# Optimization experiments

Measured on AMD Instinct MI355X. Metric: run time of the kernel, lower is better.

## Reference

```python
import jax, jax.numpy as jnp
import numpy as np

N_NODES = 50000
N_EDGES = 600000
D = 128
EDGE_D = 32
N_LAYERS = 3
BN_EPS = 1e-5


def setup_inputs() -> dict:
    key = jax.random.key(0)
    ks = jax.random.split(key, 8)
    x = jax.random.normal(ks[0], (N_NODES, D), dtype=jnp.float32)
    edge_index = jax.random.randint(ks[1], (2, N_EDGES), 0, N_NODES, dtype=jnp.int64)
    edge_attr = jax.random.normal(ks[2], (N_EDGES, EDGE_D), dtype=jnp.float32)
    W_lin = jax.random.normal(ks[3], (N_LAYERS, EDGE_D, D), dtype=jnp.float32) * 0.05
    b_lin = jnp.zeros((N_LAYERS, D), dtype=jnp.float32)
    W1 = jax.random.normal(ks[4], (N_LAYERS, D, D), dtype=jnp.float32) * 0.05
    b1 = jnp.zeros((N_LAYERS, D), dtype=jnp.float32)
    W2 = jax.random.normal(ks[5], (N_LAYERS, D, D), dtype=jnp.float32) * 0.05
    b2 = jnp.zeros((N_LAYERS, D), dtype=jnp.float32)
    gamma = jnp.ones((N_LAYERS, D), dtype=jnp.float32)
    beta = jnp.zeros((N_LAYERS, D), dtype=jnp.float32)
    return {"x": x, "edge_index": edge_index, "edge_attr": edge_attr,
            "W_lin": W_lin, "b_lin": b_lin, "W1": W1, "b1": b1,
            "W2": W2, "b2": b2, "gamma": gamma, "beta": beta}


def reference(x, edge_index, edge_attr, W_lin, b_lin, W1, b1, W2, b2, gamma, beta):
    # MPNN with GINEConv layers: for each layer,
    #   msg_e = ReLU(x[src_e] + Linear(edge_attr_e))      (PyG GINEConv edge lift)
    #   agg_i = sum over edges with dst==i of msg_e        (scatter-sum)
    #   h     = MLP((1+eps)*x + agg), eps=0
    #   x     = ReLU(BatchNorm1d(h))                       (training-mode batch stats)
    src, dst = edge_index[0], edge_index[1]
    n = x.shape[0]
    for l in range(W1.shape[0]):
        e = edge_attr @ W_lin[l] + b_lin[l]                 # [E, D]
        msg = jax.nn.relu(x[src] + e)                       # gather + fuse
        agg = jax.ops.segment_sum(msg, dst, num_segments=n)  # [N, D]
        h = x + agg                                         # eps = 0
        h = jax.nn.relu(h @ W1[l] + b1[l]) @ W2[l] + b2[l]   # GIN MLP
        mu = jnp.mean(h, axis=0)
        var = jnp.var(h, axis=0)
        h = (h - mu) * jax.lax.rsqrt(var + BN_EPS) * gamma[l] + beta[l]
        x = jax.nn.relu(h)
    return x
```

## Files before the change

kernel.cpp:

```cpp
#include <hip/hip_runtime.h>

#define D_DIM 128
#define EDGE_DIM 32
#define BN_EPS 1e-5f

typedef __attribute__((ext_vector_type(8))) _Float16 f16x8;
typedef __attribute__((ext_vector_type(2))) _Float16 half2v;
typedef __attribute__((ext_vector_type(4))) float f32x4;
typedef unsigned short ushort_t;

__device__ __forceinline__ unsigned short f2h(float f) {
    union { _Float16 h; unsigned short u; } c;
    c.h = (_Float16)f;
    return c.u;
}
__device__ __forceinline__ unsigned pk2h(float lo, float hi) {
    return (unsigned)f2h(lo) | ((unsigned)f2h(hi) << 16);
}
__device__ __forceinline__ half2v asH2(unsigned u) {
    union { unsigned u; half2v h; } c;
    c.u = u;
    return c.h;
}
__device__ __forceinline__ float fdot2f(half2v a, half2v b, float c) {
#if __has_builtin(__builtin_amdgcn_fdot2)
    return __builtin_amdgcn_fdot2(a, b, c, false);
#else
    return c + (float)a.x * (float)b.x + (float)a.y * (float)b.y;
#endif
}

__global__ __launch_bounds__(256) void hist_kernel(
    const int* __restrict__ dst, int* __restrict__ cnt, int E)
{
    for (int e = blockIdx.x * 256 + threadIdx.x; e < E; e += gridDim.x * 256)
        atomicAdd(&cnt[dst[e]], 1);
}

__global__ __launch_bounds__(256) void scan_local_kernel(
    const int* __restrict__ cnt, int* __restrict__ off,
    int* __restrict__ blksum, int n)
{
    __shared__ int part[256];
    const int t = threadIdx.x;
    const int base = blockIdx.x * 2048 + t * 8;
    int v[8];
    int s = 0;
#pragma unroll
    for (int j = 0; j < 8; ++j) {
        const int idx = base + j;
        const int c = (idx < n) ? cnt[idx] : 0;
        v[j] = s;
        s += c;
    }
    part[t] = s;
    __syncthreads();
    for (int d = 1; d < 256; d <<= 1) {
        const int val = (t >= d) ? part[t - d] : 0;
        __syncthreads();
        part[t] += val;
        __syncthreads();
    }
    const int texcl = (t > 0) ? part[t - 1] : 0;
#pragma unroll
    for (int j = 0; j < 8; ++j) {
        const int idx = base + j;
        if (idx < n) off[idx] = texcl + v[j];
    }
    if (t == 255) blksum[blockIdx.x] = part[255];
}

__global__ __launch_bounds__(64) void scan_tops_kernel(
    int* __restrict__ blksum, int* __restrict__ off, int n, int B)
{
    if (threadIdx.x == 0) {
        int run = 0;
        for (int b = 0; b < B; ++b) {
            const int v = blksum[b];
            blksum[b] = run;
            run += v;
        }
        off[n] = run;
    }
}

__global__ __launch_bounds__(256) void scan_add_kernel(
    int* __restrict__ off, int* __restrict__ cur,
    const int* __restrict__ blksum, int n)
{
    const int base = blockIdx.x * 2048;
    const int add = blksum[blockIdx.x];
    for (int j = threadIdx.x; j < 2048; j += 256) {
        const int i = base + j;
        if (i < n) {
            const int v = off[i] + add;
            off[i] = v;
            cur[i] = v;
        }
    }
}

__global__ __launch_bounds__(256) void scatter_conv_kernel(
    const int* __restrict__ src, const int* __restrict__ dst,
    const float* __restrict__ ea,
    int* __restrict__ cur, int* __restrict__ srcs,
    uint4* __restrict__ ea16q, int E)
{
    for (int e = blockIdx.x * 256 + threadIdx.x; e < E; e += gridDim.x * 256) {
        const int p = atomicAdd(&cur[dst[e]], 1);
        srcs[p] = src[e];
        const float* __restrict__ er = ea + (size_t)e * EDGE_DIM;
#pragma unroll
        for (int q = 0; q < 4; ++q) {
            const float4 a = *(const float4*)(er + q * 8);
            const float4 b = *(const float4*)(er + q * 8 + 4);
            uint4 o;
            o.x = pk2h(a.x, a.y); o.y = pk2h(a.z, a.w);
            o.z = pk2h(b.x, b.y); o.w = pk2h(b.z, b.w);
            ea16q[(size_t)p * 4 + q] = o;
        }
    }
}

__global__ __launch_bounds__(256) void wl_build_kernel(
    const float* __restrict__ Wl, unsigned* __restrict__ wl16d)
{
#pragma unroll
    for (int r = 0; r < 8; ++r) {
        const int idx = r * 256 + threadIdx.x;
        const int kp = idx >> 7, c = idx & 127;
        wl16d[idx] = pk2h(Wl[(2 * kp) * D_DIM + c], Wl[(2 * kp + 1) * D_DIM + c]);
    }
}

__global__ __launch_bounds__(256) void xprep0_kernel(
    const float* __restrict__ h, uint2* __restrict__ x16q, int M)
{
    const int total = M * 32;
    for (int i = blockIdx.x * 256 + threadIdx.x; i < total; i += gridDim.x * 256) {
        const float4 v = ((const float4*)h)[i];
        uint2 o; o.x = pk2h(v.x, v.y); o.y = pk2h(v.z, v.w);
        x16q[i] = o;
    }
}

template<int OUTF32>
__global__ __launch_bounds__(256) void apply_kernel(
    const ushort_t* __restrict__ h16, const float* __restrict__ scsh,
    uint2* __restrict__ x16q, float* __restrict__ outp, int M)
{
    __shared__ float sc[128], sh[128];
    if (threadIdx.x < 128) {
        sc[threadIdx.x] = scsh[threadIdx.x];
        sh[threadIdx.x] = scsh[128 + threadIdx.x];
    }
    __syncthreads();
    const int total = M * 32;
    for (int i = blockIdx.x * 256 + threadIdx.x; i < total; i += gridDim.x * 256) {
        const uint2 hv = *(const uint2*)(h16 + (size_t)i * 4);
        const half2v a = asH2(hv.x), b = asH2(hv.y);
        const int c = (i & 31) * 4;
        const float v0 = fmaxf(fmaf((float)a.x, sc[c + 0], sh[c + 0]), 0.f);
        const float v1 = fmaxf(fmaf((float)a.y, sc[c + 1], sh[c + 1]), 0.f);
        const float v2 = fmaxf(fmaf((float)b.x, sc[c + 2], sh[c + 2]), 0.f);
        const float v3 = fmaxf(fmaf((float)b.y, sc[c + 3], sh[c + 3]), 0.f);
        if (OUTF32) {
            f32x4 o = {v0, v1, v2, v3};
            *(f32x4*)(outp + (size_t)i * 4) = o;
        } else {
            uint2 o; o.x = pk2h(v0, v1); o.y = pk2h(v2, v3);
            x16q[i] = o;
        }
    }
}

__global__ __launch_bounds__(256) void edge_agg_kernel(
    const unsigned* __restrict__ x16d,
    const int*      __restrict__ srcs,
    const uint4*    __restrict__ ea16q,
    const int*      __restrict__ row_off,
    const unsigned* __restrict__ wl16d,
    const float*    __restrict__ bl,
    float*          __restrict__ agg,
    int nNodes)
{
    const int lane = threadIdx.x & 63;
    const int wid  = threadIdx.x >> 6;

    unsigned wA[16], wB[16];
#pragma unroll
    for (int kp = 0; kp < 16; ++kp) {
        const uint2 w2 = *(const uint2*)(wl16d + kp * 128 + 2 * lane);
        wA[kp] = w2.x; wB[kp] = w2.y;
    }
    const float b0 = bl[2 * lane];
    const float b1 = bl[2 * lane + 1];

    const int stride = gridDim.x * 4;
    for (int node = blockIdx.x * 4 + wid; node < nNodes; node += stride) {
        const int beg = __builtin_amdgcn_readfirstlane(row_off[node]);
        const int end = __builtin_amdgcn_readfirstlane(row_off[node + 1]);
        float acc0 = 0.f, acc1 = 0.f;

        auto edge_body = [&](int p) {
            const int s = srcs[p];
            const uint4 q0 = ea16q[(size_t)p * 4 + 0];
            const uint4 q1 = ea16q[(size_t)p * 4 + 1];
            const uint4 q2 = ea16q[(size_t)p * 4 + 2];
            const uint4 q3 = ea16q[(size_t)p * 4 + 3];
            const unsigned xd = x16d[(size_t)s * 64 + lane];
            const unsigned aw[16] = {q0.x, q0.y, q0.z, q0.w,
                                     q1.x, q1.y, q1.z, q1.w,
                                     q2.x, q2.y, q2.z, q2.w,
                                     q3.x, q3.y, q3.z, q3.w};
            float e0 = b0, e1 = b1;
#pragma unroll
            for (int kp = 0; kp < 16; ++kp) {
                e0 = fdot2f(asH2(aw[kp]), asH2(wA[kp]), e0);
                e1 = fdot2f(asH2(aw[kp]), asH2(wB[kp]), e1);
            }
            const half2v xh = asH2(xd);
            acc0 += fmaxf((float)xh.x + e0, 0.f);
            acc1 += fmaxf((float)xh.y + e1, 0.f);
        };

        int j = beg;
        const int head = (end - beg) & 3;
#pragma unroll 1
        for (int t = 0; t < head; ++t) { edge_body(j); ++j; }
#pragma unroll 1
        for (; j < end; j += 4) {
            edge_body(j);
            edge_body(j + 1);
            edge_body(j + 2);
            edge_body(j + 3);
        }
        *(float2*)(agg + (size_t)node * D_DIM + 2 * lane) = make_float2(acc0, acc1);
    }
}

__global__ __launch_bounds__(256) void fused_mlp_kernel(
    const unsigned* __restrict__ x16d,
    const float* __restrict__ agg,
    const float* __restrict__ W1,
    const float* __restrict__ b1,
    const float* __restrict__ W2,
    const float* __restrict__ b2,
    ushort_t* __restrict__ h16,
    float* __restrict__ sums,
    int M)
{
    __shared__ char ATb[128 * 256];
    __shared__ char WTb[128 * 256];
    __shared__ float bsum[256];
    const int tid = threadIdx.x;
    const int m0  = blockIdx.x * 128;

    bsum[tid] = 0.f;

#pragma unroll
    for (int i = 0; i < 16; ++i) {
        const int idx = i * 256 + tid;
        const int r = idx >> 5, c4 = idx & 31;
        const int row = m0 + r;
        f32x4 v = {0.f, 0.f, 0.f, 0.f};
        if (row < M) {
            const uint2 xv = *(const uint2*)(x16d + (size_t)row * 64 + c4 * 2);
            const f32x4 g  = *(const f32x4*)(agg + (size_t)row * 128 + c4 * 4);
            const half2v xa = asH2(xv.x), xb = asH2(xv.y);
            v[0] = (float)xa.x + g[0];
            v[1] = (float)xa.y + g[1];
            v[2] = (float)xb.x + g[2];
            v[3] = (float)xb.y + g[3];
        }
        uint2 p; p.x = pk2h(v[0], v[1]); p.y = pk2h(v[2], v[3]);
        *(uint2*)(ATb + r * 256 + ((c4 * 8) ^ ((r & 7) << 4))) = p;
    }
#pragma unroll
    for (int i = 0; i < 8; ++i) {
        const int c4 = (tid >> 6) + 4 * i;
        const int kp = tid & 63;
        const f32x4 wa = *(const f32x4*)(W1 + (size_t)(2 * kp) * 128 + c4 * 4);
        const f32x4 wb = *(const f32x4*)(W1 + (size_t)(2 * kp + 1) * 128 + c4 * 4);
#pragma unroll
        for (int j = 0; j < 4; ++j) {
            const int col = c4 * 4 + j;
            *(unsigned*)(WTb + col * 256 + ((kp * 4) ^ ((col & 7) << 4))) = pk2h(wa[j], wb[j]);
        }
    }
    __syncthreads();

    const int lane = tid & 63;
    const int w    = tid >> 6;
    const int fr   = lane & 15;
    const int fg   = lane >> 4;
    const int ar0  = w * 32 + fr;
    const int asz  = (ar0 & 7) << 4;

    f32x4 acc[2][8];
#pragma unroll
    for (int a = 0; a < 2; ++a)
#pragma unroll
        for (int b = 0; b < 8; ++b) acc[a][b] = (f32x4){0.f, 0.f, 0.f, 0.f};

#pragma unroll
    for (int ks = 0; ks < 4; ++ks) {
        const int kb = ks * 64 + fg * 16;
        const f16x8 a0 = *(const f16x8*)(ATb + ar0 * 256 + (kb ^ asz));
        const f16x8 a1 = *(const f16x8*)(ATb + (ar0 + 16) * 256 + (kb ^ asz));
#pragma unroll
        for (int cb = 0; cb < 8; ++cb) {
            const int col = cb * 16 + fr;
            const f16x8 b = *(const f16x8*)(WTb + col * 256 + (kb ^ ((col & 7) << 4)));
            acc[0][cb] = __builtin_amdgcn_mfma_f32_16x16x32_f16(a0, b, acc[0][cb], 0, 0, 0);
            acc[1][cb] = __builtin_amdgcn_mfma_f32_16x16x32_f16(a1, b, acc[1][cb], 0, 0, 0);
        }
    }
    __syncthreads();

    {
        float b1v[8];
#pragma unroll
        for (int cb = 0; cb < 8; ++cb) b1v[cb] = b1[cb * 16 + fr];
#pragma unroll
        for (int rf = 0; rf < 2; ++rf) {
            const int rb = w * 32 + rf * 16 + fg * 4;
#pragma unroll
            for (int cb = 0; cb < 8; ++cb) {
                const int c = cb * 16 + fr;
#pragma unroll
                for (int j = 0; j < 4; ++j) {
                    const int r = rb + j;
                    const float v = fmaxf(acc[rf][cb][j] + b1v[cb], 0.f);
                    *(ushort_t*)(ATb + r * 256 + ((c * 2) ^ ((r & 7) << 4))) = f2h(v);
                }
            }
        }
    }
#pragma unroll
    for (int i = 0; i < 8; ++i) {
        const int c4 = (tid >> 6) + 4 * i;
        const int kp = tid & 63;
        const f32x4 wa = *(const f32x4*)(W2 + (size_t)(2 * kp) * 128 + c4 * 4);
        const f32x4 wb = *(const f32x4*)(W2 + (size_t)(2 * kp + 1) * 128 + c4 * 4);
#pragma unroll
        for (int j = 0; j < 4; ++j) {
            const int col = c4 * 4 + j;
            *(unsigned*)(WTb + col * 256 + ((kp * 4) ^ ((col & 7) << 4))) = pk2h(wa[j], wb[j]);
        }
    }
#pragma unroll
    for (int a = 0; a < 2; ++a)
#pragma unroll
        for (int b = 0; b < 8; ++b) acc[a][b] = (f32x4){0.f, 0.f, 0.f, 0.f};
    __syncthreads();

#pragma unroll
    for (int ks = 0; ks < 4; ++ks) {
        const int kb = ks * 64 + fg * 16;
        const f16x8 a0 = *(const f16x8*)(ATb + ar0 * 256 + (kb ^ asz));
        const f16x8 a1 = *(const f16x8*)(ATb + (ar0 + 16) * 256 + (kb ^ asz));
#pragma unroll
        for (int cb = 0; cb < 8; ++cb) {
            const int col = cb * 16 + fr;
            const f16x8 b = *(const f16x8*)(WTb + col * 256 + (kb ^ ((col & 7) << 4)));
            acc[0][cb] = __builtin_amdgcn_mfma_f32_16x16x32_f16(a0, b, acc[0][cb], 0, 0, 0);
            acc[1][cb] = __builtin_amdgcn_mfma_f32_16x16x32_f16(a1, b, acc[1][cb], 0, 0, 0);
        }
    }

    float b2v[8];
#pragma unroll
    for (int cb = 0; cb < 8; ++cb) b2v[cb] = b2[cb * 16 + fr];
    float s[8], q[8];
#pragma unroll
    for (int cb = 0; cb < 8; ++cb) { s[cb] = 0.f; q[cb] = 0.f; }

#pragma unroll
    for (int rf = 0; rf < 2; ++rf) {
        const int r0 = m0 + w * 32 + rf * 16 + fg * 4;
#pragma unroll
        for (int cb = 0; cb < 8; ++cb) {
            const int col = cb * 16 + fr;
#pragma unroll
            for (int j = 0; j < 4; ++j) {
                const int row = r0 + j;
                if (row < M) {
                    const float v = acc[rf][cb][j] + b2v[cb];
                    h16[(size_t)row * 128 + col] = f2h(v);
                    s[cb] += v;
                    q[cb] += v * v;
                }
            }
        }
    }
#pragma unroll
    for (int cb = 0; cb < 8; ++cb) {
        float ss = s[cb]; ss += __shfl_down(ss, 32); ss += __shfl_down(ss, 16);
        float qq = q[cb]; qq += __shfl_down(qq, 32); qq += __shfl_down(qq, 16);
        if (lane < 16) {
            atomicAdd(&bsum[cb * 16 + lane], ss);
            atomicAdd(&bsum[128 + cb * 16 + lane], qq);
        }
    }
    __syncthreads();
    unsafeAtomicAdd(&sums[tid], bsum[tid]);
}

__global__ __launch_bounds__(128) void bn_finalize_kernel(
    const float* __restrict__ sums,
    const float* __restrict__ gamma, const float* __restrict__ beta,
    float* __restrict__ scsh, float invM)
{
    const int c = threadIdx.x;
    const float mu  = sums[c] * invM;
    const float var = sums[128 + c] * invM - mu * mu;
    const float sc  = gamma[c] * rsqrtf(var + BN_EPS);
    scsh[c]       = sc;
    scsh[128 + c] = beta[c] - mu * sc;
}

extern "C" void kernel_launch(void* const* d_in, const int* in_sizes, int n_in,
                              void* d_out, int out_size, void* d_ws, size_t ws_size,
                              hipStream_t stream)
{
    const float* x_in  = (const float*)d_in[0];
    const int*   ei    = (const int*)  d_in[1];
    const float* ea    = (const float*)d_in[2];
    const float* W_lin = (const float*)d_in[3];
    const float* b_lin = (const float*)d_in[4];
    const float* W1    = (const float*)d_in[5];
    const float* b1    = (const float*)d_in[6];
    const float* W2    = (const float*)d_in[7];
    const float* b2    = (const float*)d_in[8];
    const float* gamma = (const float*)d_in[9];
    const float* beta  = (const float*)d_in[10];

    const int N = in_sizes[0] / D_DIM;
    const int E = in_sizes[2] / EDGE_DIM;
    const int L = in_sizes[3] / (EDGE_DIM * D_DIM);

    const int* src = ei;
    const int* dst = ei + E;

    float* out = (float*)d_out;

    char* wp = (char*)d_ws;
    auto take = [&wp](size_t bytes) {
        char* r = wp;
        wp += (bytes + 15) & ~(size_t)15;
        return r;
    };
    float*     agg     = (float*)    take((size_t)N * D_DIM * 4);
    ushort_t*  h16     = (ushort_t*) take((size_t)N * D_DIM * 2);
    unsigned*  x16d    = (unsigned*) take((size_t)N * D_DIM * 2);
    float*     sums    = (float*)    take(256 * 4);
    float*     scsh    = (float*)    take(256 * 4);
    unsigned*  wl16d   = (unsigned*) take(16 * 128 * 4);
    int*       cnt     = (int*)      take((size_t)N * 4);
    int*       row_off = (int*)      take((size_t)(N + 1) * 4);
    int*       cur     = (int*)      take((size_t)N * 4);
    int*       blksum  = (int*)      take(256 * 4);
    int*       srcs    = (int*)      take((size_t)E * 4);
    uint4*     ea16q   = (uint4*)    take((size_t)E * 64);

    const int gemmBlocks = (N + 127) / 128;
    const int scanBlocks = (N + 2047) / 2048;

    hipMemsetAsync(cnt, 0, (size_t)N * sizeof(int), stream);
    hist_kernel<<<1024, 256, 0, stream>>>(dst, cnt, E);
    scan_local_kernel<<<scanBlocks, 256, 0, stream>>>(cnt, row_off, blksum, N);
    scan_tops_kernel<<<1, 64, 0, stream>>>(blksum, row_off, N, scanBlocks);
    scan_add_kernel<<<scanBlocks, 256, 0, stream>>>(row_off, cur, blksum, N);
    scatter_conv_kernel<<<1024, 256, 0, stream>>>(src, dst, ea, cur, srcs, ea16q, E);

    for (int l = 0; l < L; ++l) {
        hipMemsetAsync(sums, 0, 256 * sizeof(float), stream);

        const float* Wl_l = W_lin + (size_t)l * EDGE_DIM * D_DIM;
        const float* bl_l = b_lin + (size_t)l * D_DIM;
        const float* W1_l = W1 + (size_t)l * D_DIM * D_DIM;
        const float* b1_l = b1 + (size_t)l * D_DIM;
        const float* W2_l = W2 + (size_t)l * D_DIM * D_DIM;
        const float* b2_l = b2 + (size_t)l * D_DIM;

        if (l == 0)
            xprep0_kernel<<<1024, 256, 0, stream>>>(x_in, (uint2*)x16d, N);
        else
            apply_kernel<0><<<1024, 256, 0, stream>>>(h16, scsh, (uint2*)x16d, nullptr, N);

        wl_build_kernel<<<1, 256, 0, stream>>>(Wl_l, wl16d);

        edge_agg_kernel<<<2048, 256, 0, stream>>>(
            x16d, srcs, ea16q, row_off, wl16d, bl_l, agg, N);

        fused_mlp_kernel<<<gemmBlocks, 256, 0, stream>>>(
            x16d, agg, W1_l, b1_l, W2_l, b2_l, h16, sums, N);

        bn_finalize_kernel<<<1, 128, 0, stream>>>(
            sums, gamma + (size_t)l * D_DIM, beta + (size_t)l * D_DIM,
            scsh, 1.f / (float)N);
    }

    apply_kernel<1><<<1024, 256, 0, stream>>>(h16, scsh, nullptr, out, N);
}
```

Before: 433.1 us.

## Compute edge linear with MFMA per edge chunk and scatter via segmented atomics

```diff
diff --git a/kernel.cpp b/kernel.cpp
--- a/kernel.cpp
+++ b/kernel.cpp
@@ -3,6 +3,7 @@
 #define D_DIM 128
 #define EDGE_DIM 32
 #define BN_EPS 1e-5f
+#define CHUNK 128
 
 typedef __attribute__((ext_vector_type(8))) _Float16 f16x8;
 typedef __attribute__((ext_vector_type(2))) _Float16 half2v;
@@ -21,13 +22,6 @@
     union { unsigned u; half2v h; } c;
     c.u = u;
     return c.h;
-}
-__device__ __forceinline__ float fdot2f(half2v a, half2v b, float c) {
-#if __has_builtin(__builtin_amdgcn_fdot2)
-    return __builtin_amdgcn_fdot2(a, b, c, false);
-#else
-    return c + (float)a.x * (float)b.x + (float)a.y * (float)b.y;
-#endif
 }
 
 __global__ __launch_bounds__(256) void hist_kernel(
@@ -103,12 +97,14 @@
 __global__ __launch_bounds__(256) void scatter_conv_kernel(
     const int* __restrict__ src, const int* __restrict__ dst,
     const float* __restrict__ ea,
-    int* __restrict__ cur, int* __restrict__ srcs,
+    int* __restrict__ cur, int* __restrict__ srcs, int* __restrict__ dsts,
     uint4* __restrict__ ea16q, int E)
 {
     for (int e = blockIdx.x * 256 + threadIdx.x; e < E; e += gridDim.x * 256) {
-        const int p = atomicAdd(&cur[dst[e]], 1);
+        const int d = dst[e];
+        const int p = atomicAdd(&cur[d], 1);
         srcs[p] = src[e];
+        dsts[p] = d;
         const float* __restrict__ er = ea + (size_t)e * EDGE_DIM;
 #pragma unroll
         for (int q = 0; q < 4; ++q) {
@@ -122,32 +118,48 @@
     }
 }
 
-__global__ __launch_bounds__(256) void wl_build_kernel(
-    const float* __restrict__ Wl, unsigned* __restrict__ wl16d)
-{
-#pragma unroll
-    for (int r = 0; r < 8; ++r) {
-        const int idx = r * 256 + threadIdx.x;
-        const int kp = idx >> 7, c = idx & 127;
-        wl16d[idx] = pk2h(Wl[(2 * kp) * D_DIM + c], Wl[(2 * kp + 1) * D_DIM + c]);
+__global__ __launch_bounds__(256) void wbuild_kernel(
+    const float* __restrict__ Wl, const float* __restrict__ W1f,
+    const float* __restrict__ W2f,
+    unsigned* __restrict__ wflin, unsigned* __restrict__ wf1d,
+    unsigned* __restrict__ wf2d)
+{
+    const int idx = blockIdx.x * 256 + threadIdx.x;
+    if (idx < 2048) {
+        const int slot = idx >> 2, q = idx & 3;
+        const int cb = slot >> 6, lane = slot & 63;
+        const int col = cb * 16 + (lane & 15);
+        const int k0 = (lane >> 4) * 8 + 2 * q;
+        wflin[idx] = pk2h(Wl[k0 * D_DIM + col], Wl[(k0 + 1) * D_DIM + col]);
+    } else if (idx < 10240) {
+        const int i = idx - 2048;
+        const int col = i >> 6, kp = i & 63;
+        wf1d[i] = pk2h(W1f[(2 * kp) * D_DIM + col], W1f[(2 * kp + 1) * D_DIM + col]);
+    } else if (idx < 18432) {
+        const int i = idx - 10240;
+        const int col = i >> 6, kp = i & 63;
+        wf2d[i] = pk2h(W2f[(2 * kp) * D_DIM + col], W2f[(2 * kp + 1) * D_DIM + col]);
     }
 }
 
 __global__ __launch_bounds__(256) void xprep0_kernel(
-    const float* __restrict__ h, uint2* __restrict__ x16q, int M)
+    const float* __restrict__ h, uint2* __restrict__ x16q,
+    float* __restrict__ aggf, int M)
 {
     const int total = M * 32;
     for (int i = blockIdx.x * 256 + threadIdx.x; i < total; i += gridDim.x * 256) {
         const float4 v = ((const float4*)h)[i];
         uint2 o; o.x = pk2h(v.x, v.y); o.y = pk2h(v.z, v.w);
         x16q[i] = o;
+        ((float4*)aggf)[i] = v;
     }
 }
 
 template<int OUTF32>
 __global__ __launch_bounds__(256) void apply_kernel(
     const ushort_t* __restrict__ h16, const float* __restrict__ scsh,
-    uint2* __restrict__ x16q, float* __restrict__ outp, int M)
+    uint2* __restrict__ x16q, float* __restrict__ aggf,
+    float* __restrict__ outp, int M)
 {
     __shared__ float sc[128], sh[128];
     if (threadIdx.x < 128) {
@@ -170,88 +182,139 @@
         } else {
             uint2 o; o.x = pk2h(v0, v1); o.y = pk2h(v2, v3);
             x16q[i] = o;
-        }
-    }
-}
-
-__global__ __launch_bounds__(256) void edge_agg_kernel(
+            f32x4 g = {v0, v1, v2, v3};
+            *(f32x4*)(aggf + (size_t)i * 4) = g;
+        }
+    }
+}
+
+__global__ __launch_bounds__(256) void fused_edge_kernel(
     const unsigned* __restrict__ x16d,
     const int*      __restrict__ srcs,
-    const uint4*    __restrict__ ea16q,
-    const int*      __restrict__ row_off,
-    const unsigned* __restrict__ wl16d,
+    const int*      __restrict__ dsts,
+    const ushort_t* __restrict__ ea16,
+    const ushort_t* __restrict__ wflin,
     const float*    __restrict__ bl,
     float*          __restrict__ agg,
-    int nNodes)
-{
-    const int lane = threadIdx.x & 63;
-    const int wid  = threadIdx.x >> 6;
-
-    unsigned wA[16], wB[16];
-#pragma unroll
-    for (int kp = 0; kp < 16; ++kp) {
-        const uint2 w2 = *(const uint2*)(wl16d + kp * 128 + 2 * lane);
-        wA[kp] = w2.x; wB[kp] = w2.y;
-    }
-    const float b0 = bl[2 * lane];
-    const float b1 = bl[2 * lane + 1];
-
-    const int stride = gridDim.x * 4;
-    for (int node = blockIdx.x * 4 + wid; node < nNodes; node += stride) {
-        const int beg = __builtin_amdgcn_readfirstlane(row_off[node]);
-        const int end = __builtin_amdgcn_readfirstlane(row_off[node + 1]);
-        float acc0 = 0.f, acc1 = 0.f;
-
-        auto edge_body = [&](int p) {
-            const int s = srcs[p];
-            const uint4 q0 = ea16q[(size_t)p * 4 + 0];
-            const uint4 q1 = ea16q[(size_t)p * 4 + 1];
-            const uint4 q2 = ea16q[(size_t)p * 4 + 2];
-            const uint4 q3 = ea16q[(size_t)p * 4 + 3];
-            const unsigned xd = x16d[(size_t)s * 64 + lane];
-            const unsigned aw[16] = {q0.x, q0.y, q0.z, q0.w,
-                                     q1.x, q1.y, q1.z, q1.w,
-                                     q2.x, q2.y, q2.z, q2.w,
-                                     q3.x, q3.y, q3.z, q3.w};
-            float e0 = b0, e1 = b1;
-#pragma unroll
-            for (int kp = 0; kp < 16; ++kp) {
-                e0 = fdot2f(asH2(aw[kp]), asH2(wA[kp]), e0);
-                e1 = fdot2f(asH2(aw[kp]), asH2(wB[kp]), e1);
+    int E)
+{
+    __shared__ ushort_t eT[CHUNK * 132];
+    const int tid  = threadIdx.x;
+    const int lane = tid & 63;
+    const int w    = tid >> 6;
+    const int fr   = lane & 15;
+    const int fg   = lane >> 4;
+
+    f16x8 bfr[8];
+#pragma unroll
+    for (int cb = 0; cb < 8; ++cb)
+        bfr[cb] = *(const f16x8*)(wflin + (cb * 64 + lane) * 8);
+    float blv[8];
+#pragma unroll
+    for (int cb = 0; cb < 8; ++cb) blv[cb] = bl[cb * 16 + fr];
+
+    const size_t chunk0 = (size_t)blockIdx.x * CHUNK;
+#pragma unroll
+    for (int rr = 0; rr < 2; ++rr) {
+        const int rb = w * 2 + rr;
+        const f16x8 af = *(const f16x8*)(ea16 + (chunk0 + rb * 16 + fr) * 32 + fg * 8);
+        f32x4 acc[8];
+#pragma unroll
+        for (int cb = 0; cb < 8; ++cb) {
+            const f32x4 z = {0.f, 0.f, 0.f, 0.f};
+            acc[cb] = __builtin_amdgcn_mfma_f32_16x16x32_f16(af, bfr[cb], z, 0, 0, 0);
+        }
+#pragma unroll
+        for (int cb = 0; cb < 8; ++cb) {
+            const int col = cb * 16 + fr;
+#pragma unroll
+            for (int j = 0; j < 4; ++j) {
+                const int er = rb * 16 + fg * 4 + j;
+                eT[er * 132 + col] = f2h(acc[cb][j] + blv[cb]);
             }
-            const half2v xh = asH2(xd);
-            acc0 += fmaxf((float)xh.x + e0, 0.f);
-            acc1 += fmaxf((float)xh.y + e1, 0.f);
-        };
-
-        int j = beg;
-        const int head = (end - beg) & 3;
+        }
+    }
+    __syncthreads();
+
+    const int base = (int)chunk0 + w * 32;
+    int nE = E - base;
+    if (nE <= 0) return;
+    if (nE > 32) nE = 32;
+    const int pend = base + nE;
+
+    float a0 = 0.f, a1 = 0.f;
+    int p = base;
+
+    auto flush = [&](int d) {
+        unsafeAtomicAdd(&agg[(size_t)d * D_DIM + 2 * lane],     a0);
+        unsafeAtomicAdd(&agg[(size_t)d * D_DIM + 2 * lane + 1], a1);
+        a0 = 0.f; a1 = 0.f;
+    };
+
 #pragma unroll 1
-        for (int t = 0; t < head; ++t) { edge_body(j); ++j; }
+    for (; p + 3 < pend; p += 4) {
+        const int s0 = __builtin_amdgcn_readfirstlane(srcs[p]);
+        const int s1 = __builtin_amdgcn_readfirstlane(srcs[p + 1]);
+        const int s2 = __builtin_amdgcn_readfirstlane(srcs[p + 2]);
+        const int s3 = __builtin_amdgcn_readfirstlane(srcs[p + 3]);
+        const unsigned x0 = x16d[(size_t)s0 * 64 + lane];
+        const unsigned x1 = x16d[(size_t)s1 * 64 + lane];
+        const unsigned x2 = x16d[(size_t)s2 * 64 + lane];
+        const unsigned x3 = x16d[(size_t)s3 * 64 + lane];
+        const int ei = p - (int)chunk0;
+        const unsigned e0 = *(const unsigned*)&eT[(ei + 0) * 132 + 2 * lane];
+        const unsigned e1 = *(const unsigned*)&eT[(ei + 1) * 132 + 2 * lane];
+        const unsigned e2 = *(const unsigned*)&eT[(ei + 2) * 132 + 2 * lane];
+        const unsigned e3 = *(const unsigned*)&eT[(ei + 3) * 132 + 2 * lane];
+        const int d0 = __builtin_amdgcn_readfirstlane(dsts[p]);
+        const int d1 = __builtin_amdgcn_readfirstlane(dsts[p + 1]);
+        const int d2 = __builtin_amdgcn_readfirstlane(dsts[p + 2]);
+        const int d3 = __builtin_amdgcn_readfirstlane(dsts[p + 3]);
+        const int d4 = (p + 4 < pend) ? __builtin_amdgcn_readfirstlane(dsts[p + 4]) : -1;
+
+        { const half2v xh = asH2(x0), eh = asH2(e0);
+          a0 += fmaxf((float)xh.x + (float)eh.x, 0.f);
+          a1 += fmaxf((float)xh.y + (float)eh.y, 0.f);
+          if (d0 != d1) flush(d0); }
+        { const half2v xh = asH2(x1), eh = asH2(e1);
+          a0 += fmaxf((float)xh.x + (float)eh.x, 0.f);
+          a1 += fmaxf((float)xh.y + (float)eh.y, 0.f);
+          if (d1 != d2) flush(d1); }
+        { const half2v xh = asH2(x2), eh = asH2(e2);
+          a0 += fmaxf((float)xh.x + (float)eh.x, 0.f);
+          a1 += fmaxf((float)xh.y + (float)eh.y, 0.f);
+          if (d2 != d3) flush(d2); }
+        { const half2v xh = asH2(x3), eh = asH2(e3);
+          a0 += fmaxf((float)xh.x + (float)eh.x, 0.f);
+          a1 += fmaxf((float)xh.y + (float)eh.y, 0.f);
+          if (d3 != d4) flush(d3); }
+    }
 #pragma unroll 1
-        for (; j < end; j += 4) {
-            edge_body(j);
-            edge_body(j + 1);
-            edge_body(j + 2);
-            edge_body(j + 3);
-        }
-        *(float2*)(agg + (size_t)node * D_DIM + 2 * lane) = make_float2(acc0, acc1);
+    for (; p < pend; ++p) {
+        const int s = __builtin_amdgcn_readfirstlane(srcs[p]);
+        const unsigned xd = x16d[(size_t)s * 64 + lane];
+        const int ei = p - (int)chunk0;
+        const unsigned ed = *(const unsigned*)&eT[ei * 132 + 2 * lane];
+        const int d  = __builtin_amdgcn_readfirstlane(dsts[p]);
+        const int dn = (p + 1 < pend) ? __builtin_amdgcn_readfirstlane(dsts[p + 1]) : -1;
+        const half2v xh = asH2(xd), eh = asH2(ed);
+        a0 += fmaxf((float)xh.x + (float)eh.x, 0.f);
+        a1 += fmaxf((float)xh.y + (float)eh.y, 0.f);
+        if (d != dn) flush(d);
     }
 }
 
 __global__ __launch_bounds__(256) void fused_mlp_kernel(
-    const unsigned* __restrict__ x16d,
     const float* __restrict__ agg,
-    const float* __restrict__ W1,
+    const ushort_t* __restrict__ wf1,
     const float* __restrict__ b1,
-    const float* __restrict__ W2,
+    const ushort_t* __restrict__ wf2,
     const float* __restrict__ b2,
     ushort_t* __restrict__ h16,
     float* __restrict__ sums,
     int M)
 {
     __shared__ char ATb[128 * 256];
-    __shared__ char WTb[128 * 256];
     __shared__ float bsum[256];
     const int tid = threadIdx.x;
     const int m0  = blockIdx.x * 128;
@@ -264,29 +327,9 @@
         const int r = idx >> 5, c4 = idx & 31;
         const int row = m0 + r;
         f32x4 v = {0.f, 0.f, 0.f, 0.f};
-        if (row < M) {
-            const uint2 xv = *(const uint2*)(x16d + (size_t)row * 64 + c4 * 2);
-            const f32x4 g  = *(const f32x4*)(agg + (size_t)row * 128 + c4 * 4);
-            const half2v xa = asH2(xv.x), xb = asH2(xv.y);
-            v[0] = (float)xa.x + g[0];
-            v[1] = (float)xa.y + g[1];
-            v[2] = (float)xb.x + g[2];
-            v[3] = (float)xb.y + g[3];
-        }
-        uint2 p; p.x = pk2h(v[0], v[1]); p.y = pk2h(v[2], v[3]);
-        *(uint2*)(ATb + r * 256 + ((c4 * 8) ^ ((r & 7) << 4))) = p;
-    }
-#pragma unroll
-    for (int i = 0; i < 8; ++i) {
-        const int c4 = (tid >> 6) + 4 * i;
-        const int kp = tid & 63;
-        const f32x4 wa = *(const f32x4*)(W1 + (size_t)(2 * kp) * 128 + c4 * 4);
-        const f32x4 wb = *(const f32x4*)(W1 + (size_t)(2 * kp + 1) * 128 + c4 * 4);
-#pragma unroll
-        for (int j = 0; j < 4; ++j) {
-            const int col = c4 * 4 + j;
-            *(unsigned*)(WTb + col * 256 + ((kp * 4) ^ ((col & 7) << 4))) = pk2h(wa[j], wb[j]);
-        }
+        if (row < M) v = *(const f32x4*)(agg + (size_t)row * 128 + c4 * 4);
+        uint2 pk; pk.x = pk2h(v[0], v[1]); pk.y = pk2h(v[2], v[3]);
+        *(uint2*)(ATb + r * 256 + ((c4 * 8) ^ ((r & 7) << 4))) = pk;
     }
     __syncthreads();
 
@@ -308,12 +351,14 @@
         const int kb = ks * 64 + fg * 16;
         const f16x8 a0 = *(const f16x8*)(ATb + ar0 * 256 + (kb ^ asz));
         const f16x8 a1 = *(const f16x8*)(ATb + (ar0 + 16) * 256 + (kb ^ asz));
+        f16x8 bf[8];
+#pragma unroll
+        for (int cb = 0; cb < 8; ++cb)
+            bf[cb] = *(const f16x8*)(wf1 + (cb * 16 + fr) * 128 + ks * 32 + fg * 8);
 #pragma unroll
         for (int cb = 0; cb < 8; ++cb) {
-            const int col = cb * 16 + fr;
-            const f16x8 b = *(const f16x8*)(WTb + col * 256 + (kb ^ ((col & 7) << 4)));
-            acc[0][cb] = __builtin_amdgcn_mfma_f32_16x16x32_f16(a0, b, acc[0][cb], 0, 0, 0);
-            acc[1][cb] = __builtin_amdgcn_mfma_f32_16x16x32_f16(a1, b, acc[1][cb], 0, 0, 0);
+            acc[0][cb] = __builtin_amdgcn_mfma_f32_16x16x32_f16(a0, bf[cb], acc[0][cb], 0, 0, 0);
+            acc[1][cb] = __builtin_amdgcn_mfma_f32_16x16x32_f16(a1, bf[cb], acc[1][cb], 0, 0, 0);
         }
     }
     __syncthreads();
@@ -338,18 +383,6 @@
         }
     }
 #pragma unroll
-    for (int i = 0; i < 8; ++i) {
-        const int c4 = (tid >> 6) + 4 * i;
-        const int kp = tid & 63;
-        const f32x4 wa = *(const f32x4*)(W2 + (size_t)(2 * kp) * 128 + c4 * 4);
-        const f32x4 wb = *(const f32x4*)(W2 + (size_t)(2 * kp + 1) * 128 + c4 * 4);
-#pragma unroll
-        for (int j = 0; j < 4; ++j) {
-            const int col = c4 * 4 + j;
-            *(unsigned*)(WTb + col * 256 + ((kp * 4) ^ ((col & 7) << 4))) = pk2h(wa[j], wb[j]);
-        }
-    }
-#pragma unroll
     for (int a = 0; a < 2; ++a)
 #pragma unroll
         for (int b = 0; b < 8; ++b) acc[a][b] = (f32x4){0.f, 0.f, 0.f, 0.f};
@@ -360,12 +393,14 @@
         const int kb = ks * 64 + fg * 16;
         const f16x8 a0 = *(const f16x8*)(ATb + ar0 * 256 + (kb ^ asz));
         const f16x8 a1 = *(const f16x8*)(ATb + (ar0 + 16) * 256 + (kb ^ asz));
+        f16x8 bf[8];
+#pragma unroll
+        for (int cb = 0; cb < 8; ++cb)
+            bf[cb] = *(const f16x8*)(wf2 + (cb * 16 + fr) * 128 + ks * 32 + fg * 8);
 #pragma unroll
         for (int cb = 0; cb < 8; ++cb) {
-            const int col = cb * 16 + fr;
-            const f16x8 b = *(const f16x8*)(WTb + col * 256 + (kb ^ ((col & 7) << 4)));
-            acc[0][cb] = __builtin_amdgcn_mfma_f32_16x16x32_f16(a0, b, acc[0][cb], 0, 0, 0);
-            acc[1][cb] = __builtin_amdgcn_mfma_f32_16x16x32_f16(a1, b, acc[1][cb], 0, 0, 0);
+            acc[0][cb] = __builtin_amdgcn_mfma_f32_16x16x32_f16(a0, bf[cb], acc[0][cb], 0, 0, 0);
+            acc[1][cb] = __builtin_amdgcn_mfma_f32_16x16x32_f16(a1, bf[cb], acc[1][cb], 0, 0, 0);
         }
     }
 
@@ -439,6 +474,7 @@
     const int N = in_sizes[0] / D_DIM;
     const int E = in_sizes[2] / EDGE_DIM;
     const int L = in_sizes[3] / (EDGE_DIM * D_DIM);
+    const int Epad = (E + CHUNK - 1) & ~(CHUNK - 1);
 
     const int* src = ei;
     const int* dst = ei + E;
@@ -456,23 +492,27 @@
     unsigned*  x16d    = (unsigned*) take((size_t)N * D_DIM * 2);
     float*     sums    = (float*)    take(256 * 4);
     float*     scsh    = (float*)    take(256 * 4);
-    unsigned*  wl16d   = (unsigned*) take(16 * 128 * 4);
+    unsigned*  wflin   = (unsigned*) take(2048 * 4);
+    unsigned*  wf1d    = (unsigned*) take(8192 * 4);
+    unsigned*  wf2d    = (unsigned*) take(8192 * 4);
     int*       cnt     = (int*)      take((size_t)N * 4);
     int*       row_off = (int*)      take((size_t)(N + 1) * 4);
     int*       cur     = (int*)      take((size_t)N * 4);
     int*       blksum  = (int*)      take(256 * 4);
     int*       srcs    = (int*)      take((size_t)E * 4);
-    uint4*     ea16q   = (uint4*)    take((size_t)E * 64);
+    int*       dsts    = (int*)      take((size_t)E * 4);
+    uint4*     ea16q   = (uint4*)    take((size_t)Epad * 64);
 
     const int gemmBlocks = (N + 127) / 128;
     const int scanBlocks = (N + 2047) / 2048;
+    const int edgeBlocks = Epad / CHUNK;
 
     hipMemsetAsync(cnt, 0, (size_t)N * sizeof(int), stream);
     hist_kernel<<<1024, 256, 0, stream>>>(dst, cnt, E);
     scan_local_kernel<<<scanBlocks, 256, 0, stream>>>(cnt, row_off, blksum, N);
     scan_tops_kernel<<<1, 64, 0, stream>>>(blksum, row_off, N, scanBlocks);
     scan_add_kernel<<<scanBlocks, 256, 0, stream>>>(row_off, cur, blksum, N);
-    scatter_conv_kernel<<<1024, 256, 0, stream>>>(src, dst, ea, cur, srcs, ea16q, E);
+    scatter_conv_kernel<<<1024, 256, 0, stream>>>(src, dst, ea, cur, srcs, dsts, ea16q, E);
 
     for (int l = 0; l < L; ++l) {
         hipMemsetAsync(sums, 0, 256 * sizeof(float), stream);
@@ -485,22 +525,24 @@
         const float* b2_l = b2 + (size_t)l * D_DIM;
 
         if (l == 0)
-            xprep0_kernel<<<1024, 256, 0, stream>>>(x_in, (uint2*)x16d, N);
+            xprep0_kernel<<<1024, 256, 0, stream>>>(x_in, (uint2*)x16d, agg, N);
         else
-            apply_kernel<0><<<1024, 256, 0, stream>>>(h16, scsh, (uint2*)x16d, nullptr, N);
-
-        wl_build_kernel<<<1, 256, 0, stream>>>(Wl_l, wl16d);
-
-        edge_agg_kernel<<<2048, 256, 0, stream>>>(
-            x16d, srcs, ea16q, row_off, wl16d, bl_l, agg, N);
+            apply_kernel<0><<<1024, 256, 0, stream>>>(h16, scsh, (uint2*)x16d, agg, nullptr, N);
+
+        wbuild_kernel<<<72, 256, 0, stream>>>(Wl_l, W1_l, W2_l, wflin, wf1d, wf2d);
+
+        fused_edge_kernel<<<edgeBlocks, 256, 0, stream>>>(
+            x16d, srcs, dsts, (const ushort_t*)ea16q,
+            (const ushort_t*)wflin, bl_l, agg, E);
 
         fused_mlp_kernel<<<gemmBlocks, 256, 0, stream>>>(
-            x16d, agg, W1_l, b1_l, W2_l, b2_l, h16, sums, N);
+            agg, (const ushort_t*)wf1d, b1_l,
+            (const ushort_t*)wf2d, b2_l, h16, sums, N);
 
         bn_finalize_kernel<<<1, 128, 0, stream>>>(
             sums, gamma + (size_t)l * D_DIM, beta + (size_t)l * D_DIM,
             scsh, 1.f / (float)N);
     }
 
-    apply_kernel<1><<<1024, 256, 0, stream>>>(h16, scsh, nullptr, out, N);
-}
+    apply_kernel<1><<<1024, 256, 0, stream>>>(h16, scsh, nullptr, nullptr, out, N);
+}
```

Result: slower. 461.0 us (+6.4%).

## Compute edge linear with MFMA per edge chunk in LDS, emit fp16 x+agg

Applied to the files above, without the earlier changes.

```diff
diff --git a/kernel.cpp b/kernel.cpp
--- a/kernel.cpp
+++ b/kernel.cpp
@@ -3,6 +3,8 @@
 #define D_DIM 128
 #define EDGE_DIM 32
 #define BN_EPS 1e-5f
+#define CHUNK 128
+#define ECAP 192
 
 typedef __attribute__((ext_vector_type(8))) _Float16 f16x8;
 typedef __attribute__((ext_vector_type(2))) _Float16 half2v;
@@ -21,13 +23,6 @@
     union { unsigned u; half2v h; } c;
     c.u = u;
     return c.h;
-}
-__device__ __forceinline__ float fdot2f(half2v a, half2v b, float c) {
-#if __has_builtin(__builtin_amdgcn_fdot2)
-    return __builtin_amdgcn_fdot2(a, b, c, false);
-#else
-    return c + (float)a.x * (float)b.x + (float)a.y * (float)b.y;
-#endif
 }
 
 __global__ __launch_bounds__(256) void hist_kernel(
@@ -122,15 +117,28 @@
     }
 }
 
-__global__ __launch_bounds__(256) void wl_build_kernel(
-    const float* __restrict__ Wl, unsigned* __restrict__ wl16d)
-{
-#pragma unroll
-    for (int r = 0; r < 8; ++r) {
-        const int idx = r * 256 + threadIdx.x;
-        const int kp = idx >> 7, c = idx & 127;
-        wl16d[idx] = pk2h(Wl[(2 * kp) * D_DIM + c], Wl[(2 * kp + 1) * D_DIM + c]);
-    }
+__global__ __launch_bounds__(256) void chunk_first_kernel(
+    const int* __restrict__ row_off, int* __restrict__ chunk_first,
+    int n, int nchunks)
+{
+    const int i = blockIdx.x * 256 + threadIdx.x;
+    if (i == 0) chunk_first[nchunks] = n;
+    if (i < n) {
+        int c = row_off[i] >> 7;
+        if (c > nchunks - 1) c = nchunks - 1;
+        atomicMin(&chunk_first[c], i);
+    }
+}
+
+__global__ __launch_bounds__(256) void wlin_build_kernel(
+    const float* __restrict__ Wl, unsigned* __restrict__ wflin)
+{
+    const int idx = blockIdx.x * 256 + threadIdx.x;
+    const int slot = idx >> 2, q = idx & 3;
+    const int cb = slot >> 6, lane = slot & 63;
+    const int col = cb * 16 + (lane & 15);
+    const int k0 = (lane >> 4) * 8 + 2 * q;
+    wflin[idx] = pk2h(Wl[k0 * D_DIM + col], Wl[(k0 + 1) * D_DIM + col]);
 }
 
 __global__ __launch_bounds__(256) void xprep0_kernel(
@@ -174,74 +182,118 @@
     }
 }
 
-__global__ __launch_bounds__(256) void edge_agg_kernel(
+__global__ __launch_bounds__(256, 3) void fused_edge_kernel(
     const unsigned* __restrict__ x16d,
     const int*      __restrict__ srcs,
-    const uint4*    __restrict__ ea16q,
+    const ushort_t* __restrict__ ea16,
+    const ushort_t* __restrict__ wflin,
+    const float*    __restrict__ bl,
     const int*      __restrict__ row_off,
-    const unsigned* __restrict__ wl16d,
-    const float*    __restrict__ bl,
-    float*          __restrict__ agg,
+    const int*      __restrict__ chunk_first,
+    unsigned*       __restrict__ agg16d,
     int nNodes)
 {
-    const int lane = threadIdx.x & 63;
-    const int wid  = threadIdx.x >> 6;
-
-    unsigned wA[16], wB[16];
-#pragma unroll
-    for (int kp = 0; kp < 16; ++kp) {
-        const uint2 w2 = *(const uint2*)(wl16d + kp * 128 + 2 * lane);
-        wA[kp] = w2.x; wB[kp] = w2.y;
-    }
-    const float b0 = bl[2 * lane];
-    const float b1 = bl[2 * lane + 1];
-
-    const int stride = gridDim.x * 4;
-    for (int node = blockIdx.x * 4 + wid; node < nNodes; node += stride) {
-        const int beg = __builtin_amdgcn_readfirstlane(row_off[node]);
-        const int end = __builtin_amdgcn_readfirstlane(row_off[node + 1]);
-        float acc0 = 0.f, acc1 = 0.f;
-
-        auto edge_body = [&](int p) {
-            const int s = srcs[p];
-            const uint4 q0 = ea16q[(size_t)p * 4 + 0];
-            const uint4 q1 = ea16q[(size_t)p * 4 + 1];
-            const uint4 q2 = ea16q[(size_t)p * 4 + 2];
-            const uint4 q3 = ea16q[(size_t)p * 4 + 3];
-            const unsigned xd = x16d[(size_t)s * 64 + lane];
-            const unsigned aw[16] = {q0.x, q0.y, q0.z, q0.w,
-                                     q1.x, q1.y, q1.z, q1.w,
-                                     q2.x, q2.y, q2.z, q2.w,
-                                     q3.x, q3.y, q3.z, q3.w};
-            float e0 = b0, e1 = b1;
-#pragma unroll
-            for (int kp = 0; kp < 16; ++kp) {
-                e0 = fdot2f(asH2(aw[kp]), asH2(wA[kp]), e0);
-                e1 = fdot2f(asH2(aw[kp]), asH2(wB[kp]), e1);
+    __shared__ ushort_t eT[ECAP * 132];
+    const int tid  = threadIdx.x;
+    const int lane = tid & 63;
+    const int w    = tid >> 6;
+    const int fr   = lane & 15;
+    const int fg   = lane >> 4;
+    const int c    = blockIdx.x;
+
+    int nfirst = chunk_first[c];
+    int nlast  = chunk_first[c + 1];
+    if (nfirst > nNodes) nfirst = nNodes;
+    if (nlast  > nNodes) nlast  = nNodes;
+    if (nfirst >= nlast) return;
+    const int ebase = row_off[nfirst];
+    const int ecnt  = row_off[nlast] - ebase;
+
+    f16x8 bfr[8];
+#pragma unroll
+    for (int cb = 0; cb < 8; ++cb)
+        bfr[cb] = *(const f16x8*)(wflin + (cb * 64 + lane) * 8);
+    float blv[8];
+#pragma unroll
+    for (int cb = 0; cb < 8; ++cb) blv[cb] = bl[cb * 16 + fr];
+
+    const int rowblocks = (ecnt + 15) >> 4;
+#pragma unroll
+    for (int rr = 0; rr < 3; ++rr) {
+        const int rb = w + rr * 4;
+        if (rb < rowblocks) {
+            const f16x8 af = *(const f16x8*)(ea16
+                + ((size_t)(ebase + rb * 16 + fr)) * 32 + fg * 8);
+            f32x4 acc[8];
+#pragma unroll
+            for (int cb = 0; cb < 8; ++cb) {
+                const f32x4 z = {0.f, 0.f, 0.f, 0.f};
+                acc[cb] = __builtin_amdgcn_mfma_f32_16x16x32_f16(af, bfr[cb], z, 0, 0, 0);
             }
-            const half2v xh = asH2(xd);
-            acc0 += fmaxf((float)xh.x + e0, 0.f);
-            acc1 += fmaxf((float)xh.y + e1, 0.f);
-        };
-
-        int j = beg;
+#pragma unroll
+            for (int cb = 0; cb < 8; ++cb) {
+                const int col = cb * 16 + fr;
+#pragma unroll
+                for (int j = 0; j < 4; ++j) {
+                    const int er = rb * 16 + fg * 4 + j;
+                    eT[er * 132 + col] = f2h(acc[cb][j] + blv[cb]);
+                }
+            }
+        }
+    }
+    __syncthreads();
+
+    for (int n = nfirst + w; n < nlast; n += 4) {
+        const int beg = __builtin_amdgcn_readfirstlane(row_off[n]);
+        const int end = __builtin_amdgcn_readfirstlane(row_off[n + 1]);
+        float a0 = 0.f, a1 = 0.f;
+        int p = beg;
         const int head = (end - beg) & 3;
 #pragma unroll 1
-        for (int t = 0; t < head; ++t) { edge_body(j); ++j; }
+        for (int t = 0; t < head; ++t, ++p) {
+            const int s = __builtin_amdgcn_readfirstlane(srcs[p]);
+            const unsigned xd = x16d[(size_t)s * 64 + lane];
+            const unsigned ed = *(const unsigned*)&eT[(p - ebase) * 132 + 2 * lane];
+            const half2v xh = asH2(xd), eh = asH2(ed);
+            a0 += fmaxf((float)xh.x + (float)eh.x, 0.f);
+            a1 += fmaxf((float)xh.y + (float)eh.y, 0.f);
+        }
 #pragma unroll 1
-        for (; j < end; j += 4) {
-            edge_body(j);
-            edge_body(j + 1);
-            edge_body(j + 2);
-            edge_body(j + 3);
-        }
-        *(float2*)(agg + (size_t)node * D_DIM + 2 * lane) = make_float2(acc0, acc1);
+        for (; p < end; p += 4) {
+            const int s0 = __builtin_amdgcn_readfirstlane(srcs[p]);
+            const int s1 = __builtin_amdgcn_readfirstlane(srcs[p + 1]);
+            const int s2 = __builtin_amdgcn_readfirstlane(srcs[p + 2]);
+            const int s3 = __builtin_amdgcn_readfirstlane(srcs[p + 3]);
+            const unsigned x0 = x16d[(size_t)s0 * 64 + lane];
+            const unsigned x1 = x16d[(size_t)s1 * 64 + lane];
+            const unsigned x2 = x16d[(size_t)s2 * 64 + lane];
+            const unsigned x3 = x16d[(size_t)s3 * 64 + lane];
+            const int ei = p - ebase;
+            const unsigned e0 = *(const unsigned*)&eT[(ei + 0) * 132 + 2 * lane];
+            const unsigned e1 = *(const unsigned*)&eT[(ei + 1) * 132 + 2 * lane];
+            const unsigned e2 = *(const unsigned*)&eT[(ei + 2) * 132 + 2 * lane];
+            const unsigned e3 = *(const unsigned*)&eT[(ei + 3) * 132 + 2 * lane];
+            { const half2v xh = asH2(x0), eh = asH2(e0);
+              a0 += fmaxf((float)xh.x + (float)eh.x, 0.f);
+              a1 += fmaxf((float)xh.y + (float)eh.y, 0.f); }
+            { const half2v xh = asH2(x1), eh = asH2(e1);
+              a0 += fmaxf((float)xh.x + (float)eh.x, 0.f);
+              a1 += fmaxf((float)xh.y + (float)eh.y, 0.f); }
+            { const half2v xh = asH2(x2), eh = asH2(e2);
+              a0 += fmaxf((float)xh.x + (float)eh.x, 0.f);
+              a1 += fmaxf((float)xh.y + (float)eh.y, 0.f); }
+            { const half2v xh = asH2(x3), eh = asH2(e3);
+              a0 += fmaxf((float)xh.x + (float)eh.x, 0.f);
+              a1 += fmaxf((float)xh.y + (float)eh.y, 0.f); }
+        }
+        const half2v xh = asH2(x16d[(size_t)n * 64 + lane]);
+        agg16d[(size_t)n * 64 + lane] =
+            pk2h((float)xh.x + a0, (float)xh.y + a1);
     }
 }
 
 __global__ __launch_bounds__(256) void fused_mlp_kernel(
-    const unsigned* __restrict__ x16d,
-    const float* __restrict__ agg,
+    const unsigned* __restrict__ agg16d,
     const float* __restrict__ W1,
     const float* __restrict__ b1,
     const float* __restrict__ W2,
@@ -259,22 +311,13 @@
     bsum[tid] = 0.f;
 
 #pragma unroll
-    for (int i = 0; i < 16; ++i) {
+    for (int i = 0; i < 8; ++i) {
         const int idx = i * 256 + tid;
-        const int r = idx >> 5, c4 = idx & 31;
+        const int r = idx >> 4, c16 = idx & 15;
         const int row = m0 + r;
-        f32x4 v = {0.f, 0.f, 0.f, 0.f};
-        if (row < M) {
-            const uint2 xv = *(const uint2*)(x16d + (size_t)row * 64 + c4 * 2);
-            const f32x4 g  = *(const f32x4*)(agg + (size_t)row * 128 + c4 * 4);
-            const half2v xa = asH2(xv.x), xb = asH2(xv.y);
-            v[0] = (float)xa.x + g[0];
-            v[1] = (float)xa.y + g[1];
-            v[2] = (float)xb.x + g[2];
-            v[3] = (float)xb.y + g[3];
-        }
-        uint2 p; p.x = pk2h(v[0], v[1]); p.y = pk2h(v[2], v[3]);
-        *(uint2*)(ATb + r * 256 + ((c4 * 8) ^ ((r & 7) << 4))) = p;
+        uint4 v = make_uint4(0u, 0u, 0u, 0u);
+        if (row < M) v = *(const uint4*)(agg16d + (size_t)row * 64 + c16 * 4);
+        *(uint4*)(ATb + r * 256 + ((c16 * 16) ^ ((r & 7) << 4))) = v;
     }
 #pragma unroll
     for (int i = 0; i < 8; ++i) {
@@ -327,12 +370,12 @@
             const int rb = w * 32 + rf * 16 + fg * 4;
 #pragma unroll
             for (int cb = 0; cb < 8; ++cb) {
-                const int c = cb * 16 + fr;
+                const int cc = cb * 16 + fr;
 #pragma unroll
                 for (int j = 0; j < 4; ++j) {
                     const int r = rb + j;
                     const float v = fmaxf(acc[rf][cb][j] + b1v[cb], 0.f);
-                    *(ushort_t*)(ATb + r * 256 + ((c * 2) ^ ((r & 7) << 4))) = f2h(v);
+                    *(ushort_t*)(ATb + r * 256 + ((cc * 2) ^ ((r & 7) << 4))) = f2h(v);
                 }
             }
         }
@@ -439,6 +482,7 @@
     const int N = in_sizes[0] / D_DIM;
     const int E = in_sizes[2] / EDGE_DIM;
     const int L = in_sizes[3] / (EDGE_DIM * D_DIM);
+    const int nchunks = (E + CHUNK - 1) / CHUNK;
 
     const int* src = ei;
     const int* dst = ei + E;
@@ -451,27 +495,30 @@
         wp += (bytes + 15) & ~(size_t)15;
         return r;
     };
-    float*     agg     = (float*)    take((size_t)N * D_DIM * 4);
+    unsigned*  agg16d  = (unsigned*) take((size_t)N * D_DIM * 2);
     ushort_t*  h16     = (ushort_t*) take((size_t)N * D_DIM * 2);
     unsigned*  x16d    = (unsigned*) take((size_t)N * D_DIM * 2);
     float*     sums    = (float*)    take(256 * 4);
     float*     scsh    = (float*)    take(256 * 4);
-    unsigned*  wl16d   = (unsigned*) take(16 * 128 * 4);
+    unsigned*  wflin   = (unsigned*) take(2048 * 4);
     int*       cnt     = (int*)      take((size_t)N * 4);
     int*       row_off = (int*)      take((size_t)(N + 1) * 4);
     int*       cur     = (int*)      take((size_t)N * 4);
     int*       blksum  = (int*)      take(256 * 4);
+    int*       chunk1  = (int*)      take((size_t)(nchunks + 1) * 4);
     int*       srcs    = (int*)      take((size_t)E * 4);
-    uint4*     ea16q   = (uint4*)    take((size_t)E * 64);
+    uint4*     ea16q   = (uint4*)    take(((size_t)E + ECAP) * 64);
 
     const int gemmBlocks = (N + 127) / 128;
     const int scanBlocks = (N + 2047) / 2048;
 
     hipMemsetAsync(cnt, 0, (size_t)N * sizeof(int), stream);
+    hipMemsetAsync(chunk1, 0x7f, (size_t)(nchunks + 1) * sizeof(int), stream);
     hist_kernel<<<1024, 256, 0, stream>>>(dst, cnt, E);
     scan_local_kernel<<<scanBlocks, 256, 0, stream>>>(cnt, row_off, blksum, N);
     scan_tops_kernel<<<1, 64, 0, stream>>>(blksum, row_off, N, scanBlocks);
     scan_add_kernel<<<scanBlocks, 256, 0, stream>>>(row_off, cur, blksum, N);
+    chunk_first_kernel<<<(N + 255) / 256, 256, 0, stream>>>(row_off, chunk1, N, nchunks);
     scatter_conv_kernel<<<1024, 256, 0, stream>>>(src, dst, ea, cur, srcs, ea16q, E);
 
     for (int l = 0; l < L; ++l) {
@@ -489,13 +536,14 @@
         else
             apply_kernel<0><<<1024, 256, 0, stream>>>(h16, scsh, (uint2*)x16d, nullptr, N);
 
-        wl_build_kernel<<<1, 256, 0, stream>>>(Wl_l, wl16d);
-
-        edge_agg_kernel<<<2048, 256, 0, stream>>>(
-            x16d, srcs, ea16q, row_off, wl16d, bl_l, agg, N);
+        wlin_build_kernel<<<8, 256, 0, stream>>>(Wl_l, wflin);
+
+        fused_edge_kernel<<<nchunks, 256, 0, stream>>>(
+            x16d, srcs, (const ushort_t*)ea16q, (const ushort_t*)wflin,
+            bl_l, row_off, chunk1, agg16d, N);
 
         fused_mlp_kernel<<<gemmBlocks, 256, 0, stream>>>(
-            x16d, agg, W1_l, b1_l, W2_l, b2_l, h16, sums, N);
+            agg16d, W1_l, b1_l, W2_l, b2_l, h16, sums, N);
 
         bn_finalize_kernel<<<1, 128, 0, stream>>>(
             sums, gamma + (size_t)l * D_DIM, beta + (size_t)l * D_DIM,
```

Result: slower. 447.0 us (+3.2%).
